# Kernel optimization log

Hardware: AMD Instinct MI355X
Metric: run time of the kernel (lower is better)

The kernel has to match this reference:

```python
import jax, jax.numpy as jnp
import numpy as np

D_MODEL = 1024
NUM_HEADS = 16
D_K = D_MODEL // NUM_HEADS
THETA = 10000.0


def setup_inputs() -> dict:
    key = jax.random.key(0)
    ks = jax.random.split(key, 5)
    b, s = 4, 1024
    std = 1.0 / np.sqrt(D_MODEL)
    x = jax.random.normal(ks[0], (b, s, D_MODEL), dtype=jnp.float32)
    token_positions = jnp.tile(jnp.arange(s, dtype=jnp.int64)[None, :], (b, 1))
    Wq = jax.random.truncated_normal(ks[1], -3.0, 3.0, (D_MODEL, D_MODEL), jnp.float32) * std
    Wk = jax.random.truncated_normal(ks[2], -3.0, 3.0, (D_MODEL, D_MODEL), jnp.float32) * std
    Wv = jax.random.truncated_normal(ks[3], -3.0, 3.0, (D_MODEL, D_MODEL), jnp.float32) * std
    Wo = jax.random.truncated_normal(ks[4], -3.0, 3.0, (D_MODEL, D_MODEL), jnp.float32) * std
    return {"x": x, "token_positions": token_positions,
            "Wq": Wq, "Wk": Wk, "Wv": Wv, "Wo": Wo}


def _apply_rope(x):
    # x: [b, h, s, d_k]; source uses row index i (ignores token_positions)
    s, d = x.shape[-2], x.shape[-1]
    pos = jnp.arange(s, dtype=jnp.float32)                      # [s]
    kidx = jnp.arange(0, d, 2, dtype=jnp.float32)               # [d/2]
    ang = pos[:, None] / (THETA ** (kidx / d))                  # [s, d/2]
    cos, sin = jnp.cos(ang), jnp.sin(ang)
    x_even, x_odd = x[..., 0::2], x[..., 1::2]                  # [b,h,s,d/2]
    out_even = x_even * cos - x_odd * sin
    out_odd = x_even * sin + x_odd * cos
    return jnp.stack([out_even, out_odd], axis=-1).reshape(x.shape)


def reference(x, token_positions, Wq, Wk, Wv, Wo):
    b, s, _ = x.shape
    # Linear: einsum '... din, dout din -> ... dout'  => x @ W.T
    q = jnp.einsum('bsd,ed->bse', x, Wq)
    k = jnp.einsum('bsd,ed->bse', x, Wk)
    v = jnp.einsum('bsd,ed->bse', x, Wv)
    # split heads -> [b, h, s, d_k]
    def split(t):
        return t.reshape(b, s, NUM_HEADS, D_K).transpose(0, 2, 1, 3)
    q, k, v = split(q), split(k), split(v)
    q = _apply_rope(q)
    k = _apply_rope(k)
    scores = jnp.einsum('bhqd,bhkd->bhqk', q, k) / np.sqrt(D_K)
    causal = jnp.tril(jnp.ones((s, s), dtype=bool))
    scores = jnp.where(causal, scores, -jnp.inf)
    attn = jax.nn.softmax(scores, axis=-1)
    out = jnp.einsum('bhqk,bhkd->bhqd', attn, v)
    out = out.transpose(0, 2, 1, 3).reshape(b, s, D_MODEL)
    return jnp.einsum('bsd,ed->bse', out, Wo)
```

## Files before the change

### kernel.cpp

```cpp
#include <hip/hip_runtime.h>

typedef __attribute__((ext_vector_type(8))) short short8;
typedef __attribute__((ext_vector_type(8))) __bf16 bf16x8;
typedef __attribute__((ext_vector_type(4))) float f32x4;
typedef __attribute__((ext_vector_type(4))) float float4v;
typedef __attribute__((ext_vector_type(4))) unsigned short ushort4v;
typedef __attribute__((ext_vector_type(2))) unsigned uint2v;

#define AS1 __attribute__((address_space(1)))
#define AS3 __attribute__((address_space(3)))

#define BATCH 4
#define SEQ 1024
#define DM 1024
#define NH 16
#define DKH 64
#define MROWS (BATCH * SEQ)
#define N3 (3 * DM)

static __device__ __forceinline__ unsigned short f2bf(float f) {
  unsigned u = __builtin_bit_cast(unsigned, f);
  u += 0x7FFFu + ((u >> 16) & 1u);
  return (unsigned short)(u >> 16);
}
static __device__ __forceinline__ float bf2f(unsigned short h) {
  return __builtin_bit_cast(float, ((unsigned)h) << 16);
}
static __device__ __forceinline__ f32x4 mfma16(short8 a, short8 b, f32x4 c) {
  return __builtin_amdgcn_mfma_f32_16x16x32_bf16(
      __builtin_bit_cast(bf16x8, a), __builtin_bit_cast(bf16x8, b), c, 0, 0, 0);
}

__global__ __launch_bounds__(256) void convert_kernel(
    const float* __restrict__ x, const float* __restrict__ wq,
    const float* __restrict__ wk, const float* __restrict__ wv,
    const float* __restrict__ wo, unsigned short* __restrict__ xb,
    unsigned short* __restrict__ wqkv, unsigned short* __restrict__ wob) {
  size_t i4 = ((size_t)blockIdx.x * 256 + threadIdx.x) * 4;
  const size_t SZX = (size_t)MROWS * DM;
  const size_t SZW = (size_t)DM * DM;
  const float* src;
  unsigned short* dst;
  size_t off;
  if (i4 < SZX) {
    src = x; dst = xb; off = i4;
  } else if (i4 < SZX + SZW) {
    src = wq; dst = wqkv; off = i4 - SZX;
  } else if (i4 < SZX + 2 * SZW) {
    src = wk; dst = wqkv + SZW; off = i4 - SZX - SZW;
  } else if (i4 < SZX + 3 * SZW) {
    src = wv; dst = wqkv + 2 * SZW; off = i4 - SZX - 2 * SZW;
  } else {
    src = wo; dst = wob; off = i4 - SZX - 3 * SZW;
  }
  float4v v = *(const float4v*)(src + off);
  ushort4v o;
  o.x = f2bf(v.x); o.y = f2bf(v.y); o.z = f2bf(v.z); o.w = f2bf(v.w);
  *(ushort4v*)(dst + off) = o;
}

static __device__ __forceinline__ void store_c(float* p, float v) { *p = v; }
static __device__ __forceinline__ void store_c(unsigned short* p, float v) { *p = f2bf(v); }

template <typename OutT>
__global__ __launch_bounds__(256) void gemm_bt(
    const unsigned short* __restrict__ A, const unsigned short* __restrict__ B,
    OutT* __restrict__ C, int M, int N, int K) {
  __shared__ char sA[16384];
  __shared__ char sB[16384];
  const int tid = threadIdx.x, w = tid >> 6, lane = tid & 63;
  const int g = lane >> 4, r = lane & 15;
  const int m0 = blockIdx.y * 128, n0 = blockIdx.x * 128;
  const int wm = (w >> 1) * 64, wn = (w & 1) * 64;
  f32x4 acc[4][4] = {};
  for (int k0 = 0; k0 < K; k0 += 64) {
#pragma unroll
    for (int c = 0; c < 4; ++c) {
      int p = c * 4096 + tid * 16;
      int o = p ^ (((p >> 7) & 7) << 4);
      int row = o >> 7, colb = o & 127;
      const char* ga = (const char*)(A + (size_t)(m0 + row) * K + k0) + colb;
      const char* gb = (const char*)(B + (size_t)(n0 + row) * K + k0) + colb;
      __builtin_amdgcn_global_load_lds((const AS1 void*)ga,
                                       (AS3 void*)(sA + c * 4096 + (w << 10)), 16, 0, 0);
      __builtin_amdgcn_global_load_lds((const AS1 void*)gb,
                                       (AS3 void*)(sB + c * 4096 + (w << 10)), 16, 0, 0);
    }
    __syncthreads();
#pragma unroll
    for (int kk = 0; kk < 2; ++kk) {
      short8 af[4], bfr[4];
#pragma unroll
      for (int i = 0; i < 4; ++i) {
        int ra = wm + i * 16 + r;
        af[i] = *(const short8*)(sA + (((ra << 7) + (kk << 6) + (g << 4)) ^ ((ra & 7) << 4)));
        int rb = wn + i * 16 + r;
        bfr[i] = *(const short8*)(sB + (((rb << 7) + (kk << 6) + (g << 4)) ^ ((rb & 7) << 4)));
      }
#pragma unroll
      for (int i = 0; i < 4; ++i)
#pragma unroll
        for (int j = 0; j < 4; ++j) acc[i][j] = mfma16(af[i], bfr[j], acc[i][j]);
    }
    __syncthreads();
  }
#pragma unroll
  for (int i = 0; i < 4; ++i)
#pragma unroll
    for (int j = 0; j < 4; ++j)
#pragma unroll
      for (int jj = 0; jj < 4; ++jj) {
        int row = m0 + wm + i * 16 + g * 4 + jj;
        int col = n0 + wn + j * 16 + r;
        store_c(&C[(size_t)row * N + col], acc[i][j][jj]);
      }
}

__global__ __launch_bounds__(256) void rope_qk(const unsigned short* __restrict__ cf,
                                               unsigned short* __restrict__ qb,
                                               unsigned short* __restrict__ kb) {
  int i = blockIdx.x * 256 + threadIdx.x;
  int k = i & 31, h = (i >> 5) & 15, s = (i >> 9) & 1023, b = i >> 19;
  float freq = __expf(-(float)k * 0.28782313662425572f);
  float ang = (float)s * freq;
  float sn, cs;
  __sincosf(ang, &sn, &cs);
  const unsigned short* src = cf + (size_t)(b * SEQ + s) * N3 + h * DKH + 2 * k;
  float qe = bf2f(src[0]), qo = bf2f(src[1]);
  float ke = bf2f(src[DM]), ko = bf2f(src[DM + 1]);
  float q0 = (qe * cs - qo * sn) * 0.125f;
  float q1 = (qe * sn + qo * cs) * 0.125f;
  float k0 = ke * cs - ko * sn;
  float k1 = ke * sn + ko * cs;
  size_t dsto = (size_t)((b * NH + h) * SEQ + s) * DKH + 2 * k;
  *(unsigned*)(qb + dsto) = (unsigned)f2bf(q0) | ((unsigned)f2bf(q1) << 16);
  *(unsigned*)(kb + dsto) = (unsigned)f2bf(k0) | ((unsigned)f2bf(k1) << 16);
}

__global__ __launch_bounds__(256) void transpose_v(const unsigned short* __restrict__ cf,
                                                   unsigned short* __restrict__ vt) {
  __shared__ unsigned short tile[64][72];
  int bh = blockIdx.y, b = bh >> 4, h = bh & 15, s0 = blockIdx.x * 64;
  int t = threadIdx.x, row = t >> 2, c0 = (t & 3) * 16;
  const unsigned short* src = cf + (size_t)(b * SEQ + s0 + row) * N3 + 2 * DM + h * DKH + c0;
  short8 v0 = *(const short8*)src;
  short8 v1 = *(const short8*)(src + 8);
  *(short8*)&tile[row][c0] = v0;
  *(short8*)&tile[row][c0 + 8] = v1;
  __syncthreads();
  unsigned short* dst = vt + ((size_t)bh * DKH + row) * SEQ + s0 + c0;
  short8 o0, o1;
#pragma unroll
  for (int j = 0; j < 8; ++j) o0[j] = (short)tile[c0 + j][row];
#pragma unroll
  for (int j = 0; j < 8; ++j) o1[j] = (short)tile[c0 + 8 + j][row];
  *(short8*)dst = o0;
  *(short8*)(dst + 8) = o1;
}

__global__ __launch_bounds__(128) void attn_kernel(const unsigned short* __restrict__ qb,
                                                   const unsigned short* __restrict__ kb,
                                                   const unsigned short* __restrict__ vt,
                                                   unsigned short* __restrict__ ob) {
  __shared__ char kl[2][8192];
  __shared__ char vl[2][8192];
  __shared__ unsigned short plds[2][2][1024];
  const int bx = blockIdx.x, bh = blockIdx.y, b = bh >> 4, h = bh & 15;
  const int qtlo = bx, qthi = 31 - bx;
  const int tid = threadIdx.x, w = tid >> 6, lane = tid & 63;
  const int g = lane >> 4, r = lane & 15;
  const unsigned short* Q = qb + (size_t)bh * SEQ * DKH;
  const char* Kp = (const char*)(kb + (size_t)bh * SEQ * DKH);
  const char* Vp = (const char*)(vt + (size_t)bh * DKH * SEQ);

  int pc0 = tid * 16;
  size_t ks[4], vs[4];
#pragma unroll
  for (int c = 0; c < 4; ++c) {
    int p = c * 2048 + pc0;
    int o = p ^ (((p >> 7) & 7) << 4);
    int row = o >> 7, colb = o & 127;
    ks[c] = (size_t)row * 128 + colb;
    vs[c] = (size_t)row * 2048 + colb;
  }

#define STAGE_KV(bi, kt)                                                          \
  do {                                                                            \
    const char* kbase = Kp + (size_t)(kt) * 8192;                                 \
    const char* vbase = Vp + (size_t)(kt) * 128;                                  \
    _Pragma("unroll") for (int c = 0; c < 4; ++c) {                               \
      __builtin_amdgcn_global_load_lds((const AS1 void*)(kbase + ks[c]),          \
                                       (AS3 void*)(kl[bi] + c * 2048 + pc0), 16,  \
                                       0, 0);                                     \
      __builtin_amdgcn_global_load_lds((const AS1 void*)(vbase + vs[c]),          \
                                       (AS3 void*)(vl[bi] + c * 2048 + pc0), 16,  \
                                       0, 0);                                     \
    }                                                                             \
  } while (0)

  short8 qfL0, qfL1, qfH0, qfH1;
  {
    int qrL = qtlo * 32 + w * 16 + r;
    int qrH = qthi * 32 + w * 16 + r;
    qfL0 = *(const short8*)(Q + (size_t)qrL * DKH + g * 8);
    qfL1 = *(const short8*)(Q + (size_t)qrL * DKH + 32 + g * 8);
    qfH0 = *(const short8*)(Q + (size_t)qrH * DKH + g * 8);
    qfH1 = *(const short8*)(Q + (size_t)qrH * DKH + 32 + g * 8);
  }
  f32x4 oaccL[4] = {}, oaccH[4] = {};
  float mrunL = -1e30f, lrunL = 0.f, mrunH = -1e30f, lrunH = 0.f;
  const int qgH = qthi * 32 + w * 16 + r;
  const int qgL = qtlo * 32 + w * 16 + r;
  char* pbH = (char*)&plds[w][0][0];
  char* pbL = (char*)&plds[w][1][0];
  const int nktH = (qthi + 2) >> 1;
  const int nktL = (qtlo + 2) >> 1;

  STAGE_KV(0, 0);
  __syncthreads();

  for (int kt = 0; kt < nktH; ++kt) {
    if (kt + 1 < nktH) STAGE_KV((kt + 1) & 1, kt + 1);
    const bool doLo = (kt < nktL);
    const char* kb_ = kl[kt & 1];
    const char* vb_ = vl[kt & 1];
    f32x4 sh[4] = {}, sl[4] = {};
#pragma unroll
    for (int nb = 0; nb < 4; ++nb) {
      int ra = nb * 16 + r;
      short8 kf0 = *(const short8*)(kb_ + ((ra * 128 + g * 16) ^ ((ra & 7) << 4)));
      short8 kf1 = *(const short8*)(kb_ + ((ra * 128 + 64 + g * 16) ^ ((ra & 7) << 4)));
      sh[nb] = mfma16(kf0, qfH0, sh[nb]);
      sh[nb] = mfma16(kf1, qfH1, sh[nb]);
      if (doLo) {
        sl[nb] = mfma16(kf0, qfL0, sl[nb]);
        sl[nb] = mfma16(kf1, qfL1, sl[nb]);
      }
    }
    if (kt == nktH - 1) {
#pragma unroll
      for (int nb = 0; nb < 4; ++nb)
#pragma unroll
        for (int j = 0; j < 4; ++j)
          if (kt * 64 + nb * 16 + g * 4 + j > qgH) sh[nb][j] = -1e30f;
    }
    if (doLo && kt == nktL - 1) {
#pragma unroll
      for (int nb = 0; nb < 4; ++nb)
#pragma unroll
        for (int j = 0; j < 4; ++j)
          if (kt * 64 + nb * 16 + g * 4 + j > qgL) sl[nb][j] = -1e30f;
    }
    float sclH, sclL = 1.f;
    {
      float a0 = fmaxf(fmaxf(sh[0][0], sh[0][1]), fmaxf(sh[0][2], sh[0][3]));
      float a1 = fmaxf(fmaxf(sh[1][0], sh[1][1]), fmaxf(sh[1][2], sh[1][3]));
      float a2 = fmaxf(fmaxf(sh[2][0], sh[2][1]), fmaxf(sh[2][2], sh[2][3]));
      float a3 = fmaxf(fmaxf(sh[3][0], sh[3][1]), fmaxf(sh[3][2], sh[3][3]));
      float tm = fmaxf(fmaxf(a0, a1), fmaxf(a2, a3));
      tm = fmaxf(tm, __shfl_xor(tm, 16, 64));
      tm = fmaxf(tm, __shfl_xor(tm, 32, 64));
      float mnew = fmaxf(mrunH, tm);
      sclH = __expf(mrunH - mnew);
      mrunH = mnew;
      float ps = 0.f;
#pragma unroll
      for (int nb = 0; nb < 4; ++nb)
#pragma unroll
        for (int j = 0; j < 4; ++j) {
          float p = __expf(sh[nb][j] - mnew);
          sh[nb][j] = p;
          ps += p;
        }
      ps += __shfl_xor(ps, 16, 64);
      ps += __shfl_xor(ps, 32, 64);
      lrunH = lrunH * sclH + ps;
#pragma unroll
      for (int nb = 0; nb < 4; ++nb) {
        uint2v pk;
        pk.x = (unsigned)f2bf(sh[nb][0]) | ((unsigned)f2bf(sh[nb][1]) << 16);
        pk.y = (unsigned)f2bf(sh[nb][2]) | ((unsigned)f2bf(sh[nb][3]) << 16);
        *(uint2v*)(pbH + ((r * 128 + nb * 32 + g * 8) ^ ((r & 7) << 4))) = pk;
      }
    }
    if (doLo) {
      float a0 = fmaxf(fmaxf(sl[0][0], sl[0][1]), fmaxf(sl[0][2], sl[0][3]));
      float a1 = fmaxf(fmaxf(sl[1][0], sl[1][1]), fmaxf(sl[1][2], sl[1][3]));
      float a2 = fmaxf(fmaxf(sl[2][0], sl[2][1]), fmaxf(sl[2][2], sl[2][3]));
      float a3 = fmaxf(fmaxf(sl[3][0], sl[3][1]), fmaxf(sl[3][2], sl[3][3]));
      float tm = fmaxf(fmaxf(a0, a1), fmaxf(a2, a3));
      tm = fmaxf(tm, __shfl_xor(tm, 16, 64));
      tm = fmaxf(tm, __shfl_xor(tm, 32, 64));
      float mnew = fmaxf(mrunL, tm);
      sclL = __expf(mrunL - mnew);
      mrunL = mnew;
      float ps = 0.f;
#pragma unroll
      for (int nb = 0; nb < 4; ++nb)
#pragma unroll
        for (int j = 0; j < 4; ++j) {
          float p = __expf(sl[nb][j] - mnew);
          sl[nb][j] = p;
          ps += p;
        }
      ps += __shfl_xor(ps, 16, 64);
      ps += __shfl_xor(ps, 32, 64);
      lrunL = lrunL * sclL + ps;
#pragma unroll
      for (int nb = 0; nb < 4; ++nb) {
        uint2v pk;
        pk.x = (unsigned)f2bf(sl[nb][0]) | ((unsigned)f2bf(sl[nb][1]) << 16);
        pk.y = (unsigned)f2bf(sl[nb][2]) | ((unsigned)f2bf(sl[nb][3]) << 16);
        *(uint2v*)(pbL + ((r * 128 + nb * 32 + g * 8) ^ ((r & 7) << 4))) = pk;
      }
    }
#pragma unroll
    for (int db = 0; db < 4; ++db) {
      f32x4 t = oaccH[db];
      t[0] *= sclH; t[1] *= sclH; t[2] *= sclH; t[3] *= sclH;
      oaccH[db] = t;
      if (doLo) {
        f32x4 u = oaccL[db];
        u[0] *= sclL; u[1] *= sclL; u[2] *= sclL; u[3] *= sclL;
        oaccL[db] = u;
      }
    }
    asm volatile("s_waitcnt lgkmcnt(0)" ::: "memory");
    __builtin_amdgcn_sched_barrier(0);
    short8 pfH0 = *(const short8*)(pbH + ((r * 128 + g * 16) ^ ((r & 7) << 4)));
    short8 pfH1 = *(const short8*)(pbH + ((r * 128 + 64 + g * 16) ^ ((r & 7) << 4)));
    short8 pfL0, pfL1;
    if (doLo) {
      pfL0 = *(const short8*)(pbL + ((r * 128 + g * 16) ^ ((r & 7) << 4)));
      pfL1 = *(const short8*)(pbL + ((r * 128 + 64 + g * 16) ^ ((r & 7) << 4)));
    }
#pragma unroll
    for (int db = 0; db < 4; ++db) {
      int rv = db * 16 + r;
      short8 vf0 = *(const short8*)(vb_ + ((rv * 128 + g * 16) ^ ((rv & 7) << 4)));
      short8 vf1 = *(const short8*)(vb_ + ((rv * 128 + 64 + g * 16) ^ ((rv & 7) << 4)));
      oaccH[db] = mfma16(vf0, pfH0, oaccH[db]);
      oaccH[db] = mfma16(vf1, pfH1, oaccH[db]);
      if (doLo) {
        oaccL[db] = mfma16(vf0, pfL0, oaccL[db]);
        oaccL[db] = mfma16(vf1, pfL1, oaccL[db]);
      }
    }
    __syncthreads();
  }
  {
    float invH = 1.f / lrunH;
    unsigned short* orH = ob + (size_t)(b * SEQ + qgH) * DM + h * DKH;
#pragma unroll
    for (int db = 0; db < 4; ++db) {
      uint2v pk;
      pk.x = (unsigned)f2bf(oaccH[db][0] * invH) | ((unsigned)f2bf(oaccH[db][1] * invH) << 16);
      pk.y = (unsigned)f2bf(oaccH[db][2] * invH) | ((unsigned)f2bf(oaccH[db][3] * invH) << 16);
      *(uint2v*)(orH + db * 16 + g * 4) = pk;
    }
    float invL = 1.f / lrunL;
    unsigned short* orL = ob + (size_t)(b * SEQ + qgL) * DM + h * DKH;
#pragma unroll
    for (int db = 0; db < 4; ++db) {
      uint2v pk;
      pk.x = (unsigned)f2bf(oaccL[db][0] * invL) | ((unsigned)f2bf(oaccL[db][1] * invL) << 16);
      pk.y = (unsigned)f2bf(oaccL[db][2] * invL) | ((unsigned)f2bf(oaccL[db][3] * invL) << 16);
      *(uint2v*)(orL + db * 16 + g * 4) = pk;
    }
  }
#undef STAGE_KV
}

extern "C" void kernel_launch(void* const* d_in, const int* in_sizes, int n_in,
                              void* d_out, int out_size, void* d_ws, size_t ws_size,
                              hipStream_t stream) {
  const float* x = (const float*)d_in[0];
  const float* wq = (const float*)d_in[2];
  const float* wk = (const float*)d_in[3];
  const float* wv = (const float*)d_in[4];
  const float* wo = (const float*)d_in[5];
  char* ws = (char*)d_ws;
  unsigned short* xb = (unsigned short*)(ws);
  unsigned short* wqkv = (unsigned short*)(ws + (8u << 20));
  unsigned short* wob = (unsigned short*)(ws + (14u << 20));
  unsigned short* cf = (unsigned short*)(ws + (16u << 20));
  unsigned short* qbuf = (unsigned short*)(ws + (40u << 20));
  unsigned short* kbuf = (unsigned short*)(ws + (48u << 20));
  unsigned short* vtb = (unsigned short*)(ws + (56u << 20));
  unsigned short* obuf = (unsigned short*)(ws + (64u << 20));
  float* out = (float*)d_out;

  convert_kernel<<<8192, 256, 0, stream>>>(x, wq, wk, wv, wo, xb, wqkv, wob);
  gemm_bt<unsigned short><<<dim3(24, 32), 256, 0, stream>>>(xb, wqkv, cf, MROWS, N3, DM);
  rope_qk<<<8192, 256, 0, stream>>>(cf, qbuf, kbuf);
  transpose_v<<<dim3(16, 64), 256, 0, stream>>>(cf, vtb);
  attn_kernel<<<dim3(16, 64), 128, 0, stream>>>(qbuf, kbuf, vtb, obuf);
  gemm_bt<float><<<dim3(8, 32), 256, 0, stream>>>(obuf, wob, out, MROWS, DM, DM);
}
```

Baseline: 118.3 us.

## Restructure attention into 4-wave blocks with 128-key tiles and direct V loads

The attention kernel now runs 256-thread blocks, each covering 64-row query tiles paired low/high, and processes 128 keys per iteration instead of 64. Only K is staged into LDS through global_load_lds. V fragments are read directly from global memory inside the PV loop, which removes V staging. s_setprio raises wave priority around the MFMA sections. The aim is to cut loop iterations and sync overhead and to free LDS, at the cost of uncached global V reads that may add latency and more register pressure.

```diff
diff --git a/kernel.cpp b/kernel.cpp
--- a/kernel.cpp
+++ b/kernel.cpp
@@ -158,50 +158,43 @@
   *(short8*)(dst + 8) = o1;
 }
 
-__global__ __launch_bounds__(128) void attn_kernel(const unsigned short* __restrict__ qb,
-                                                   const unsigned short* __restrict__ kb,
-                                                   const unsigned short* __restrict__ vt,
-                                                   unsigned short* __restrict__ ob) {
-  __shared__ char kl[2][8192];
-  __shared__ char vl[2][8192];
-  __shared__ unsigned short plds[2][2][1024];
+__global__ __launch_bounds__(256, 2) void attn_kernel(const unsigned short* __restrict__ qb,
+                                                      const unsigned short* __restrict__ kb,
+                                                      const unsigned short* __restrict__ vt,
+                                                      unsigned short* __restrict__ ob) {
+  __shared__ char kl[2][16384];
+  __shared__ unsigned short plds[4][2][2048];
   const int bx = blockIdx.x, bh = blockIdx.y, b = bh >> 4, h = bh & 15;
-  const int qtlo = bx, qthi = 31 - bx;
+  const int qlo = bx, qhi = 15 - bx;
   const int tid = threadIdx.x, w = tid >> 6, lane = tid & 63;
   const int g = lane >> 4, r = lane & 15;
   const unsigned short* Q = qb + (size_t)bh * SEQ * DKH;
   const char* Kp = (const char*)(kb + (size_t)bh * SEQ * DKH);
   const char* Vp = (const char*)(vt + (size_t)bh * DKH * SEQ);
 
-  int pc0 = tid * 16;
-  size_t ks[4], vs[4];
+  const int pc0 = tid * 16;
+  size_t ks[4];
 #pragma unroll
   for (int c = 0; c < 4; ++c) {
-    int p = c * 2048 + pc0;
+    int p = c * 4096 + pc0;
     int o = p ^ (((p >> 7) & 7) << 4);
-    int row = o >> 7, colb = o & 127;
-    ks[c] = (size_t)row * 128 + colb;
-    vs[c] = (size_t)row * 2048 + colb;
-  }
-
-#define STAGE_KV(bi, kt)                                                          \
+    ks[c] = (size_t)(o >> 7) * 128 + (o & 127);
+  }
+
+#define STAGE_K(bi, kt)                                                           \
   do {                                                                            \
-    const char* kbase = Kp + (size_t)(kt) * 8192;                                 \
-    const char* vbase = Vp + (size_t)(kt) * 128;                                  \
+    const char* kbase = Kp + (size_t)(kt) * 16384;                                \
     _Pragma("unroll") for (int c = 0; c < 4; ++c) {                               \
       __builtin_amdgcn_global_load_lds((const AS1 void*)(kbase + ks[c]),          \
-                                       (AS3 void*)(kl[bi] + c * 2048 + pc0), 16,  \
-                                       0, 0);                                     \
-      __builtin_amdgcn_global_load_lds((const AS1 void*)(vbase + vs[c]),          \
-                                       (AS3 void*)(vl[bi] + c * 2048 + pc0), 16,  \
+                                       (AS3 void*)(kl[bi] + c * 4096 + pc0), 16,  \
                                        0, 0);                                     \
     }                                                                             \
   } while (0)
 
   short8 qfL0, qfL1, qfH0, qfH1;
   {
-    int qrL = qtlo * 32 + w * 16 + r;
-    int qrH = qthi * 32 + w * 16 + r;
+    int qrL = qlo * 64 + w * 16 + r;
+    int qrH = qhi * 64 + w * 16 + r;
     qfL0 = *(const short8*)(Q + (size_t)qrL * DKH + g * 8);
     qfL1 = *(const short8*)(Q + (size_t)qrL * DKH + 32 + g * 8);
     qfH0 = *(const short8*)(Q + (size_t)qrH * DKH + g * 8);
@@ -209,24 +202,24 @@
   }
   f32x4 oaccL[4] = {}, oaccH[4] = {};
   float mrunL = -1e30f, lrunL = 0.f, mrunH = -1e30f, lrunH = 0.f;
-  const int qgH = qthi * 32 + w * 16 + r;
-  const int qgL = qtlo * 32 + w * 16 + r;
+  const int qgH = qhi * 64 + w * 16 + r;
+  const int qgL = qlo * 64 + w * 16 + r;
   char* pbH = (char*)&plds[w][0][0];
   char* pbL = (char*)&plds[w][1][0];
-  const int nktH = (qthi + 2) >> 1;
-  const int nktL = (qtlo + 2) >> 1;
-
-  STAGE_KV(0, 0);
+  const int nktH = (qhi + 2) >> 1;
+  const int nktL = (qlo + 2) >> 1;
+
+  STAGE_K(0, 0);
   __syncthreads();
 
   for (int kt = 0; kt < nktH; ++kt) {
-    if (kt + 1 < nktH) STAGE_KV((kt + 1) & 1, kt + 1);
+    if (kt + 1 < nktH) STAGE_K((kt + 1) & 1, kt + 1);
     const bool doLo = (kt < nktL);
     const char* kb_ = kl[kt & 1];
-    const char* vb_ = vl[kt & 1];
-    f32x4 sh[4] = {}, sl[4] = {};
-#pragma unroll
-    for (int nb = 0; nb < 4; ++nb) {
+    f32x4 sh[8] = {}, sl[8] = {};
+    __builtin_amdgcn_s_setprio(1);
+#pragma unroll
+    for (int nb = 0; nb < 8; ++nb) {
       int ra = nb * 16 + r;
       short8 kf0 = *(const short8*)(kb_ + ((ra * 128 + g * 16) ^ ((ra & 7) << 4)));
       short8 kf1 = *(const short8*)(kb_ + ((ra * 128 + 64 + g * 16) ^ ((ra & 7) << 4)));
@@ -237,27 +230,27 @@
         sl[nb] = mfma16(kf1, qfL1, sl[nb]);
       }
     }
+    __builtin_amdgcn_s_setprio(0);
     if (kt == nktH - 1) {
 #pragma unroll
-      for (int nb = 0; nb < 4; ++nb)
+      for (int nb = 0; nb < 8; ++nb)
 #pragma unroll
         for (int j = 0; j < 4; ++j)
-          if (kt * 64 + nb * 16 + g * 4 + j > qgH) sh[nb][j] = -1e30f;
+          if (kt * 128 + nb * 16 + g * 4 + j > qgH) sh[nb][j] = -1e30f;
     }
     if (doLo && kt == nktL - 1) {
 #pragma unroll
-      for (int nb = 0; nb < 4; ++nb)
+      for (int nb = 0; nb < 8; ++nb)
 #pragma unroll
         for (int j = 0; j < 4; ++j)
-          if (kt * 64 + nb * 16 + g * 4 + j > qgL) sl[nb][j] = -1e30f;
+          if (kt * 128 + nb * 16 + g * 4 + j > qgL) sl[nb][j] = -1e30f;
     }
     float sclH, sclL = 1.f;
     {
-      float a0 = fmaxf(fmaxf(sh[0][0], sh[0][1]), fmaxf(sh[0][2], sh[0][3]));
-      float a1 = fmaxf(fmaxf(sh[1][0], sh[1][1]), fmaxf(sh[1][2], sh[1][3]));
-      float a2 = fmaxf(fmaxf(sh[2][0], sh[2][1]), fmaxf(sh[2][2], sh[2][3]));
-      float a3 = fmaxf(fmaxf(sh[3][0], sh[3][1]), fmaxf(sh[3][2], sh[3][3]));
-      float tm = fmaxf(fmaxf(a0, a1), fmaxf(a2, a3));
+      float tm = -1e30f;
+#pragma unroll
+      for (int nb = 0; nb < 8; ++nb)
+        tm = fmaxf(tm, fmaxf(fmaxf(sh[nb][0], sh[nb][1]), fmaxf(sh[nb][2], sh[nb][3])));
       tm = fmaxf(tm, __shfl_xor(tm, 16, 64));
       tm = fmaxf(tm, __shfl_xor(tm, 32, 64));
       float mnew = fmaxf(mrunH, tm);
@@ -265,7 +258,7 @@
       mrunH = mnew;
       float ps = 0.f;
 #pragma unroll
-      for (int nb = 0; nb < 4; ++nb)
+      for (int nb = 0; nb < 8; ++nb)
 #pragma unroll
         for (int j = 0; j < 4; ++j) {
           float p = __expf(sh[nb][j] - mnew);
@@ -276,19 +269,18 @@
       ps += __shfl_xor(ps, 32, 64);
       lrunH = lrunH * sclH + ps;
 #pragma unroll
-      for (int nb = 0; nb < 4; ++nb) {
+      for (int nb = 0; nb < 8; ++nb) {
         uint2v pk;
         pk.x = (unsigned)f2bf(sh[nb][0]) | ((unsigned)f2bf(sh[nb][1]) << 16);
         pk.y = (unsigned)f2bf(sh[nb][2]) | ((unsigned)f2bf(sh[nb][3]) << 16);
-        *(uint2v*)(pbH + ((r * 128 + nb * 32 + g * 8) ^ ((r & 7) << 4))) = pk;
+        *(uint2v*)(pbH + ((r * 256 + nb * 32 + g * 8) ^ ((r & 7) << 4))) = pk;
       }
     }
     if (doLo) {
-      float a0 = fmaxf(fmaxf(sl[0][0], sl[0][1]), fmaxf(sl[0][2], sl[0][3]));
-      float a1 = fmaxf(fmaxf(sl[1][0], sl[1][1]), fmaxf(sl[1][2], sl[1][3]));
-      float a2 = fmaxf(fmaxf(sl[2][0], sl[2][1]), fmaxf(sl[2][2], sl[2][3]));
-      float a3 = fmaxf(fmaxf(sl[3][0], sl[3][1]), fmaxf(sl[3][2], sl[3][3]));
-      float tm = fmaxf(fmaxf(a0, a1), fmaxf(a2, a3));
+      float tm = -1e30f;
+#pragma unroll
+      for (int nb = 0; nb < 8; ++nb)
+        tm = fmaxf(tm, fmaxf(fmaxf(sl[nb][0], sl[nb][1]), fmaxf(sl[nb][2], sl[nb][3])));
       tm = fmaxf(tm, __shfl_xor(tm, 16, 64));
       tm = fmaxf(tm, __shfl_xor(tm, 32, 64));
       float mnew = fmaxf(mrunL, tm);
@@ -296,7 +288,7 @@
       mrunL = mnew;
       float ps = 0.f;
 #pragma unroll
-      for (int nb = 0; nb < 4; ++nb)
+      for (int nb = 0; nb < 8; ++nb)
 #pragma unroll
         for (int j = 0; j < 4; ++j) {
           float p = __expf(sl[nb][j] - mnew);
@@ -307,11 +299,11 @@
       ps += __shfl_xor(ps, 32, 64);
       lrunL = lrunL * sclL + ps;
 #pragma unroll
-      for (int nb = 0; nb < 4; ++nb) {
+      for (int nb = 0; nb < 8; ++nb) {
         uint2v pk;
         pk.x = (unsigned)f2bf(sl[nb][0]) | ((unsigned)f2bf(sl[nb][1]) << 16);
         pk.y = (unsigned)f2bf(sl[nb][2]) | ((unsigned)f2bf(sl[nb][3]) << 16);
-        *(uint2v*)(pbL + ((r * 128 + nb * 32 + g * 8) ^ ((r & 7) << 4))) = pk;
+        *(uint2v*)(pbL + ((r * 256 + nb * 32 + g * 8) ^ ((r & 7) << 4))) = pk;
       }
     }
 #pragma unroll
@@ -327,25 +319,25 @@
     }
     asm volatile("s_waitcnt lgkmcnt(0)" ::: "memory");
     __builtin_amdgcn_sched_barrier(0);
-    short8 pfH0 = *(const short8*)(pbH + ((r * 128 + g * 16) ^ ((r & 7) << 4)));
-    short8 pfH1 = *(const short8*)(pbH + ((r * 128 + 64 + g * 16) ^ ((r & 7) << 4)));
-    short8 pfL0, pfL1;
-    if (doLo) {
-      pfL0 = *(const short8*)(pbL + ((r * 128 + g * 16) ^ ((r & 7) << 4)));
-      pfL1 = *(const short8*)(pbL + ((r * 128 + 64 + g * 16) ^ ((r & 7) << 4)));
-    }
+    short8 pfH[4], pfL[4];
+#pragma unroll
+    for (int kss = 0; kss < 4; ++kss) {
+      pfH[kss] = *(const short8*)(pbH + ((r * 256 + kss * 64 + g * 16) ^ ((r & 7) << 4)));
+      if (doLo)
+        pfL[kss] = *(const short8*)(pbL + ((r * 256 + kss * 64 + g * 16) ^ ((r & 7) << 4)));
+    }
+    __builtin_amdgcn_s_setprio(1);
 #pragma unroll
     for (int db = 0; db < 4; ++db) {
-      int rv = db * 16 + r;
-      short8 vf0 = *(const short8*)(vb_ + ((rv * 128 + g * 16) ^ ((rv & 7) << 4)));
-      short8 vf1 = *(const short8*)(vb_ + ((rv * 128 + 64 + g * 16) ^ ((rv & 7) << 4)));
-      oaccH[db] = mfma16(vf0, pfH0, oaccH[db]);
-      oaccH[db] = mfma16(vf1, pfH1, oaccH[db]);
-      if (doLo) {
-        oaccL[db] = mfma16(vf0, pfL0, oaccL[db]);
-        oaccL[db] = mfma16(vf1, pfL1, oaccL[db]);
-      }
-    }
+      const char* vrow = Vp + (size_t)(db * 16 + r) * 2048 + (size_t)kt * 256 + g * 16;
+#pragma unroll
+      for (int kss = 0; kss < 4; ++kss) {
+        short8 vf = *(const short8*)(vrow + kss * 64);
+        oaccH[db] = mfma16(vf, pfH[kss], oaccH[db]);
+        if (doLo) oaccL[db] = mfma16(vf, pfL[kss], oaccL[db]);
+      }
+    }
+    __builtin_amdgcn_s_setprio(0);
     __syncthreads();
   }
   {
@@ -368,7 +360,7 @@
       *(uint2v*)(orL + db * 16 + g * 4) = pk;
     }
   }
-#undef STAGE_KV
+#undef STAGE_K
 }
 
 extern "C" void kernel_launch(void* const* d_in, const int* in_sizes, int n_in,
@@ -394,6 +386,6 @@
   gemm_bt<unsigned short><<<dim3(24, 32), 256, 0, stream>>>(xb, wqkv, cf, MROWS, N3, DM);
   rope_qk<<<8192, 256, 0, stream>>>(cf, qbuf, kbuf);
   transpose_v<<<dim3(16, 64), 256, 0, stream>>>(cf, vtb);
-  attn_kernel<<<dim3(16, 64), 128, 0, stream>>>(qbuf, kbuf, vtb, obuf);
+  attn_kernel<<<dim3(8, 64), 256, 0, stream>>>(qbuf, kbuf, vtb, obuf);
   gemm_bt<float><<<dim3(8, 32), 256, 0, stream>>>(obuf, wob, out, MROWS, DM, DM);
 }
```

New measurement: 192.4 us. +62.6%, slower.
